# Performance work log

Hardware: AMD Instinct MI355X
Metric: run time of the kernel (lower is better)

## Reference

```python
import jax, jax.numpy as jnp
import numpy as np

B, N, D, DEG = 1, 1024, 64, 64
K = 1.0  # Lorentz curvature parameter


def _ln(x, eps=1e-6):
    mu = jnp.mean(x, -1, keepdims=True)
    var = jnp.var(x, -1, keepdims=True)
    return (x - mu) / jnp.sqrt(var + eps)


def setup_inputs() -> dict:
    key = jax.random.key(0)
    ks = jax.random.split(key, 8)
    # valid Lorentz points: time = sqrt(||space||^2 + K)
    xs = jax.random.normal(ks[0], (B, N, D - 1), dtype=jnp.float32)
    x0 = jnp.sqrt(jnp.sum(xs ** 2, -1, keepdims=True) + K)
    x = jnp.concatenate([x0, xs], -1)
    # deterministic adjacency: node i -> (i+1..i+DEG) mod N, exactly E=N*DEG edges
    rows = np.repeat(np.arange(N), DEG)
    cols = (rows + np.tile(np.arange(1, DEG + 1), N)) % N
    adj_np = np.zeros((B, N, N), dtype=bool)
    adj_np[0, rows, cols] = True
    adj = jnp.asarray(adj_np)
    e = jax.random.normal(ks[1], (B, N, N, D), dtype=jnp.float32) * 0.1
    def lin(k, fo, fi):
        return jax.random.normal(k, (fo, fi), dtype=jnp.float32) / np.sqrt(fi).astype(np.float32)
    return dict(
        x=x, adj=adj, e=e, num_edges=B * N * DEG,
        W_edge=lin(ks[2], D, 3 * D), b_edge=jnp.zeros((D,), jnp.float32),
        W_node=lin(ks[3], D, 2 * D), b_node=jnp.zeros((D,), jnp.float32),
        W_hyp=lin(ks[4], D - 1, D), b_hyp=jnp.zeros((D - 1,), jnp.float32),
        W_ada=lin(ks[5], 2 * D, 1), b_ada=jnp.zeros((2 * D,), jnp.float32),
        W_adan=lin(ks[6], 3 * D, D), b_adan=jnp.zeros((3 * D,), jnp.float32),
    )


def reference(x, adj, e, num_edges, W_edge, b_edge, W_node, b_node, W_hyp, b_hyp, W_ada, b_ada, W_adan, b_adan):
    Bx, Nx, Dx = x.shape
    # manifold.logmap0 at origin o=(sqrt(K),0,..): tangent has time component 0
    x0 = x[..., :1]
    xs = x[..., 1:]
    xn = jnp.maximum(jnp.linalg.norm(xs, axis=-1, keepdims=True), 1e-7)
    u = jnp.sqrt(K) * jnp.arccosh(jnp.maximum(x0 / jnp.sqrt(K), 1.0 + 1e-7)) * xs / xn
    xt = jnp.concatenate([jnp.zeros_like(x0), u], -1)  # [B,N,D]
    # edge list (static size)
    bi, ii, jj = jnp.nonzero(adj, size=num_edges)
    hi = xt[bi, ii]          # [E,D]
    hj = xt[bi, jj]          # [E,D]
    ef = e[bi, ii, jj]       # [E,D]
    # Lorentz distance, per-edge (same math as dense cdist + gather)
    inner = -hi[:, 0] * hj[:, 0] + jnp.sum(hi[:, 1:] * hj[:, 1:], -1)
    dist = jnp.clip(jnp.sqrt(K) * jnp.arccosh(jnp.maximum(-inner / K, 1.0 + 1e-7)), 1e-6, 100.0)
    # adaLN modulation from distance: SiLU -> Linear(1, 2D)
    ada = jax.nn.silu(dist[:, None]) @ W_ada.T + b_ada      # [E,2D]
    shift, scale = jnp.split(ada, 2, axis=1)
    ei = jnp.concatenate([hi, hj, ef], -1) @ W_edge.T + b_edge  # [E,D]
    efu = _ln(ei) * (1.0 + scale) + shift                   # [E,D]
    # node model: scatter-mean by source node index into B*N slots (faithful)
    xf = xt.reshape(Bx * Nx, Dx)
    agg = jax.ops.segment_sum(efu, ii, num_segments=Bx * Nx)
    cnt = jax.ops.segment_sum(jnp.ones_like(dist), ii, num_segments=Bx * Nx)
    agg = agg / jnp.maximum(cnt, 1.0)[:, None]
    adan = jax.nn.silu(agg) @ W_adan.T + b_adan             # [B*N,3D]
    sh, sc, gate = jnp.split(adan, 3, axis=1)
    h = xf + gate * (_ln(jnp.concatenate([xf, agg], -1) @ W_node.T + b_node) * (1.0 + sc) + sh)
    # LorentzHypLinear: project space then recompute time
    sp = h @ W_hyp.T + b_hyp                                # [B*N,D-1]
    t = jnp.sqrt(jnp.sum(sp ** 2, -1, keepdims=True) + K)
    out = jnp.concatenate([t, sp], -1) * jnp.sqrt(K / K)    # manifold_out.k == manifold.k
    return out.reshape(Bx, Nx, Dx)
```

## Files before the change

kernel.cpp:

```cpp
#include <hip/hip_runtime.h>

#define N_NODES 1024
#define D 64
#define FSTRIDE 200

typedef __bf16 bf16x8 __attribute__((ext_vector_type(8)));
typedef __bf16 bf16x4 __attribute__((ext_vector_type(4)));
typedef float f32x4 __attribute__((ext_vector_type(4)));

__device__ __forceinline__ float wave_reduce_sum(float v) {
#pragma unroll
    for (int m = 32; m >= 1; m >>= 1) v += __shfl_xor(v, m, 64);
    return v;
}

__global__ __launch_bounds__(256) void prep_kernel(const float* __restrict__ W_edge,
                                                   __bf16* __restrict__ Wb) {
    int idx = blockIdx.x * 256 + threadIdx.x;
    float4 v = ((const float4*)W_edge)[idx];
    bf16x4 o = {(__bf16)v.x, (__bf16)v.y, (__bf16)v.z, (__bf16)v.w};
    ((bf16x4*)Wb)[idx] = o;
}

__global__ __launch_bounds__(64) void xt_kernel(const float* __restrict__ x,
                                                float* __restrict__ xt) {
    const int i = blockIdx.x;
    const int l = threadIdx.x;
    float v = x[i * D + l];
    float s = (l >= 1) ? v * v : 0.f;
    s = wave_reduce_sum(s);
    float xn = fmaxf(sqrtf(s), 1e-7f);
    float x0 = __shfl(v, 0, 64);
    float z = fmaxf(x0, 1.0f + 1e-7f);
    float ach = logf(z + sqrtf((z - 1.f) * (z + 1.f)));
    float u = (l >= 1) ? ach * v / xn : 0.f;
    xt[i * D + l] = u;
}

__global__ __launch_bounds__(256) void node_kernel(
    const float* __restrict__ xt, const float* __restrict__ eg,
    const __bf16* __restrict__ Wb, const float* __restrict__ b_edge,
    const float* __restrict__ W_node, const float* __restrict__ b_node,
    const float* __restrict__ W_hyp, const float* __restrict__ b_hyp,
    const float* __restrict__ W_ada, const float* __restrict__ b_ada,
    const float* __restrict__ W_adan, const float* __restrict__ b_adan,
    float* __restrict__ out) {
    __shared__ __align__(16) char smem[27392];
    __bf16* s_F = (__bf16*)smem;
    float* s_wada = (float*)(smem + 25600);
    float* s_bada = (float*)(smem + 26112);
    float* s_sd   = (float*)(smem + 26624);
    float* s_hi   = (float*)(smem + 26880);
    float* s_be   = (float*)(smem + 27136);
    float* s_aggw = (float*)smem;
    float* s_agg  = (float*)(smem + 1024);
    float* s_sagg = (float*)(smem + 1280);
    float* s_adan = (float*)(smem + 1536);
    float* s_h    = (float*)(smem + 2304);

    const int i = blockIdx.x;
    const int t = threadIdx.x;
    const int w = t >> 6;
    const int l = t & 63;
    const int m = l & 15;
    const int q = l >> 4;

    if (t < 128) { s_wada[t] = W_ada[t]; s_bada[t] = b_ada[t]; }
    if (t < 64)  { s_hi[t] = xt[i * D + t]; s_be[t] = b_edge[t]; }

    const float hvf = xt[i * D + l];
    const __bf16 hib = (__bf16)hvf;
    float prod[16];
#pragma unroll
    for (int el = 0; el < 16; ++el) {
        int e = w * 16 + el;
        int j = (i + e + 1) & (N_NODES - 1);
        float hjv = xt[j * D + l];
        float efv = eg[((size_t)i * N_NODES + j) * D + l];
        prod[el] = hvf * hjv;
        s_F[e * FSTRIDE + l]       = hib;
        s_F[e * FSTRIDE + 64 + l]  = (__bf16)hjv;
        s_F[e * FSTRIDE + 128 + l] = (__bf16)efv;
    }
#pragma unroll
    for (int el = 0; el < 16; ++el) {
#pragma unroll
        for (int msk = 32; msk >= 1; msk >>= 1)
            prod[el] += __shfl_xor(prod[el], msk, 64);
    }
#pragma unroll
    for (int el = 0; el < 16; ++el) {
        float zz = fmaxf(-prod[el], 1.0f + 1e-7f);
        float dist = logf(zz + sqrtf((zz - 1.f) * (zz + 1.f)));
        dist = fminf(fmaxf(dist, 1e-6f), 100.f);
        float sdv = dist / (1.f + expf(-dist));
        if (l == el) s_sd[w * 16 + el] = sdv;
    }
    __syncthreads();

    f32x4 acc[4] = {};
    const bf16x8* Arow = (const bf16x8*)(s_F + (w * 16 + m) * FSTRIDE);
    const bf16x8* Wb8 = (const bf16x8*)Wb;
#pragma unroll
    for (int ks = 0; ks < 6; ++ks) {
        bf16x8 af = Arow[ks * 4 + q];
#pragma unroll
        for (int nt = 0; nt < 4; ++nt) {
            bf16x8 bfr = Wb8[(nt * 16 + m) * 24 + ks * 4 + q];
            acc[nt] = __builtin_amdgcn_mfma_f32_16x16x32_bf16(af, bfr, acc[nt], 0, 0, 0);
        }
    }
    __syncthreads();

    float vv[4][4];
    float s1[4] = {0.f, 0.f, 0.f, 0.f}, s2[4] = {0.f, 0.f, 0.f, 0.f};
#pragma unroll
    for (int nt = 0; nt < 4; ++nt) {
        float be = s_be[nt * 16 + m];
#pragma unroll
        for (int r = 0; r < 4; ++r) {
            float x = acc[nt][r] + be;
            vv[nt][r] = x;
            s1[r] += x;
            s2[r] += x * x;
        }
    }
#pragma unroll
    for (int msk = 1; msk <= 8; msk <<= 1) {
#pragma unroll
        for (int r = 0; r < 4; ++r) {
            s1[r] += __shfl_xor(s1[r], msk, 64);
            s2[r] += __shfl_xor(s2[r], msk, 64);
        }
    }
    float colp[4] = {0.f, 0.f, 0.f, 0.f};
#pragma unroll
    for (int r = 0; r < 4; ++r) {
        float mu = s1[r] * (1.f / 64.f);
        float var = s2[r] * (1.f / 64.f) - mu * mu;
        float inv = 1.f / sqrtf(var + 1e-6f);
        float sd = s_sd[w * 16 + q * 4 + r];
#pragma unroll
        for (int nt = 0; nt < 4; ++nt) {
            int n = nt * 16 + m;
            float ln = (vv[nt][r] - mu) * inv;
            float scale = sd * s_wada[64 + n] + s_bada[64 + n];
            float shift = sd * s_wada[n] + s_bada[n];
            colp[nt] += ln * (1.f + scale) + shift;
        }
    }
#pragma unroll
    for (int nt = 0; nt < 4; ++nt) {
        colp[nt] += __shfl_xor(colp[nt], 16, 64);
        colp[nt] += __shfl_xor(colp[nt], 32, 64);
    }
    if (q == 0) {
#pragma unroll
        for (int nt = 0; nt < 4; ++nt) s_aggw[w * 64 + nt * 16 + m] = colp[nt];
    }
    __syncthreads();

    if (t < 64) {
        float agg = (s_aggw[t] + s_aggw[64 + t] + s_aggw[128 + t] + s_aggw[192 + t]) * (1.f / 64.f);
        s_agg[t] = agg;
        s_sagg[t] = agg / (1.f + expf(-agg));
    }
    __syncthreads();

    if (t < 192) {
        float a = b_adan[t];
        const float4* wr = (const float4*)(W_adan + t * 64);
#pragma unroll
        for (int k = 0; k < 16; ++k) {
            float4 wv = wr[k];
            a += wv.x * s_sagg[4 * k] + wv.y * s_sagg[4 * k + 1] +
                 wv.z * s_sagg[4 * k + 2] + wv.w * s_sagg[4 * k + 3];
        }
        s_adan[t] = a;
    }
    __syncthreads();

    if (w == 0) {
        float nv = b_node[l];
        const float4* wr = (const float4*)(W_node + l * 128);
#pragma unroll
        for (int k = 0; k < 16; ++k) {
            float4 wv = wr[k];
            nv += wv.x * s_hi[4 * k] + wv.y * s_hi[4 * k + 1] +
                  wv.z * s_hi[4 * k + 2] + wv.w * s_hi[4 * k + 3];
        }
#pragma unroll
        for (int k = 16; k < 32; ++k) {
            float4 wv = wr[k];
            int b = 4 * (k - 16);
            nv += wv.x * s_agg[b] + wv.y * s_agg[b + 1] +
                  wv.z * s_agg[b + 2] + wv.w * s_agg[b + 3];
        }
        float r1 = wave_reduce_sum(nv);
        float r2 = wave_reduce_sum(nv * nv);
        float mu = r1 * (1.f / 64.f);
        float var = r2 * (1.f / 64.f) - mu * mu;
        float ln = (nv - mu) / sqrtf(var + 1e-6f);
        float sh = s_adan[l], sc = s_adan[64 + l], gate = s_adan[128 + l];
        float h = s_hi[l] + gate * (ln * (1.f + sc) + sh);
        s_h[l] = h;

        float sp = 0.f;
        if (l >= 1) {
            const float4* wr2 = (const float4*)(W_hyp + (l - 1) * 64);
            sp = b_hyp[l - 1];
#pragma unroll
            for (int k = 0; k < 16; ++k) {
                float4 wv = wr2[k];
                sp += wv.x * s_h[4 * k] + wv.y * s_h[4 * k + 1] +
                      wv.z * s_h[4 * k + 2] + wv.w * s_h[4 * k + 3];
            }
        }
        float ss = wave_reduce_sum(sp * sp);
        float tt = sqrtf(ss + 1.0f);
        out[i * D + l] = (l == 0) ? tt : sp;
    }
}

extern "C" void kernel_launch(void* const* d_in, const int* in_sizes, int n_in,
                              void* d_out, int out_size, void* d_ws, size_t ws_size,
                              hipStream_t stream) {
    const float* x      = (const float*)d_in[0];
    const float* eg     = (const float*)d_in[2];
    const float* W_edge = (const float*)d_in[4];
    const float* b_edge = (const float*)d_in[5];
    const float* W_node = (const float*)d_in[6];
    const float* b_node = (const float*)d_in[7];
    const float* W_hyp  = (const float*)d_in[8];
    const float* b_hyp  = (const float*)d_in[9];
    const float* W_ada  = (const float*)d_in[10];
    const float* b_ada  = (const float*)d_in[11];
    const float* W_adan = (const float*)d_in[12];
    const float* b_adan = (const float*)d_in[13];
    float*  xt = (float*)d_ws;
    __bf16* Wb = (__bf16*)((char*)d_ws + 262144);

    prep_kernel<<<12, 256, 0, stream>>>(W_edge, Wb);
    xt_kernel<<<N_NODES, 64, 0, stream>>>(x, xt);
    node_kernel<<<N_NODES, 256, 0, stream>>>(xt, eg, Wb, b_edge, W_node, b_node,
                                             W_hyp, b_hyp, W_ada, b_ada, W_adan, b_adan,
                                             (float*)d_out);
}
```

Baseline: 353.4 us.

## Hoist per-node hi projection out of edge GEMM and fuse weight prep into xt kernel

Because hi is identical for all 64 edges of a node, its contribution W_edge[:, :64]·hi is computed once per block as a bias vector, and the MFMA GEMM shrinks from K=192 to K=128. This reduces shared-memory staging per edge row and the LDS footprint, which may allow more resident blocks. The W_edge-to-bf16 conversion is merged into the xt kernel, removing one launch. The hi contribution is now computed in fp32 scalar code using bf16 weights and an fp32 hi, so rounding differs slightly from before.

```diff
diff --git a/kernel.cpp b/kernel.cpp
--- a/kernel.cpp
+++ b/kernel.cpp
@@ -2,7 +2,7 @@
 
 #define N_NODES 1024
 #define D 64
-#define FSTRIDE 200
+#define FSTRIDE 136
 
 typedef __bf16 bf16x8 __attribute__((ext_vector_type(8)));
 typedef __bf16 bf16x4 __attribute__((ext_vector_type(4)));
@@ -14,18 +14,21 @@
     return v;
 }
 
-__global__ __launch_bounds__(256) void prep_kernel(const float* __restrict__ W_edge,
-                                                   __bf16* __restrict__ Wb) {
-    int idx = blockIdx.x * 256 + threadIdx.x;
-    float4 v = ((const float4*)W_edge)[idx];
-    bf16x4 o = {(__bf16)v.x, (__bf16)v.y, (__bf16)v.z, (__bf16)v.w};
-    ((bf16x4*)Wb)[idx] = o;
-}
-
 __global__ __launch_bounds__(64) void xt_kernel(const float* __restrict__ x,
-                                                float* __restrict__ xt) {
+                                                float* __restrict__ xt,
+                                                const float* __restrict__ W_edge,
+                                                __bf16* __restrict__ Wb) {
     const int i = blockIdx.x;
     const int l = threadIdx.x;
+    if (i < 12) {
+#pragma unroll
+        for (int r = 0; r < 4; ++r) {
+            int idx = i * 256 + r * 64 + l;
+            float4 v = ((const float4*)W_edge)[idx];
+            bf16x4 o = {(__bf16)v.x, (__bf16)v.y, (__bf16)v.z, (__bf16)v.w};
+            ((bf16x4*)Wb)[idx] = o;
+        }
+    }
     float v = x[i * D + l];
     float s = (l >= 1) ? v * v : 0.f;
     s = wave_reduce_sum(s);
@@ -45,13 +48,13 @@
     const float* __restrict__ W_ada, const float* __restrict__ b_ada,
     const float* __restrict__ W_adan, const float* __restrict__ b_adan,
     float* __restrict__ out) {
-    __shared__ __align__(16) char smem[27392];
+    __shared__ __align__(16) char smem[19456];
     __bf16* s_F = (__bf16*)smem;
-    float* s_wada = (float*)(smem + 25600);
-    float* s_bada = (float*)(smem + 26112);
-    float* s_sd   = (float*)(smem + 26624);
-    float* s_hi   = (float*)(smem + 26880);
-    float* s_be   = (float*)(smem + 27136);
+    float* s_wada = (float*)(smem + 17408);
+    float* s_bada = (float*)(smem + 17920);
+    float* s_sd   = (float*)(smem + 18432);
+    float* s_hi   = (float*)(smem + 18688);
+    float* s_base = (float*)(smem + 18944);
     float* s_aggw = (float*)smem;
     float* s_agg  = (float*)(smem + 1024);
     float* s_sagg = (float*)(smem + 1280);
@@ -66,10 +69,9 @@
     const int q = l >> 4;
 
     if (t < 128) { s_wada[t] = W_ada[t]; s_bada[t] = b_ada[t]; }
-    if (t < 64)  { s_hi[t] = xt[i * D + t]; s_be[t] = b_edge[t]; }
+    if (t < 64)  s_hi[t] = xt[i * D + t];
 
     const float hvf = xt[i * D + l];
-    const __bf16 hib = (__bf16)hvf;
     float prod[16];
 #pragma unroll
     for (int el = 0; el < 16; ++el) {
@@ -78,9 +80,19 @@
         float hjv = xt[j * D + l];
         float efv = eg[((size_t)i * N_NODES + j) * D + l];
         prod[el] = hvf * hjv;
-        s_F[e * FSTRIDE + l]       = hib;
-        s_F[e * FSTRIDE + 64 + l]  = (__bf16)hjv;
-        s_F[e * FSTRIDE + 128 + l] = (__bf16)efv;
+        s_F[e * FSTRIDE + l]      = (__bf16)hjv;
+        s_F[e * FSTRIDE + 64 + l] = (__bf16)efv;
+    }
+    if (t < 64) {
+        float acc = b_edge[t];
+        const bf16x8* wrow = (const bf16x8*)(Wb + t * 192);
+#pragma unroll
+        for (int c = 0; c < 8; ++c) {
+            bf16x8 wv = wrow[c];
+#pragma unroll
+            for (int j8 = 0; j8 < 8; ++j8) acc += (float)wv[j8] * s_hi[c * 8 + j8];
+        }
+        s_base[t] = acc;
     }
 #pragma unroll
     for (int el = 0; el < 16; ++el) {
@@ -102,11 +114,11 @@
     const bf16x8* Arow = (const bf16x8*)(s_F + (w * 16 + m) * FSTRIDE);
     const bf16x8* Wb8 = (const bf16x8*)Wb;
 #pragma unroll
-    for (int ks = 0; ks < 6; ++ks) {
+    for (int ks = 0; ks < 4; ++ks) {
         bf16x8 af = Arow[ks * 4 + q];
 #pragma unroll
         for (int nt = 0; nt < 4; ++nt) {
-            bf16x8 bfr = Wb8[(nt * 16 + m) * 24 + ks * 4 + q];
+            bf16x8 bfr = Wb8[(nt * 16 + m) * 24 + 8 + ks * 4 + q];
             acc[nt] = __builtin_amdgcn_mfma_f32_16x16x32_bf16(af, bfr, acc[nt], 0, 0, 0);
         }
     }
@@ -116,7 +128,7 @@
     float s1[4] = {0.f, 0.f, 0.f, 0.f}, s2[4] = {0.f, 0.f, 0.f, 0.f};
 #pragma unroll
     for (int nt = 0; nt < 4; ++nt) {
-        float be = s_be[nt * 16 + m];
+        float be = s_base[nt * 16 + m];
 #pragma unroll
         for (int r = 0; r < 4; ++r) {
             float x = acc[nt][r] + be;
@@ -240,8 +252,7 @@
     float*  xt = (float*)d_ws;
     __bf16* Wb = (__bf16*)((char*)d_ws + 262144);
 
-    prep_kernel<<<12, 256, 0, stream>>>(W_edge, Wb);
-    xt_kernel<<<N_NODES, 64, 0, stream>>>(x, xt);
+    xt_kernel<<<N_NODES, 64, 0, stream>>>(x, xt, W_edge, Wb);
     node_kernel<<<N_NODES, 256, 0, stream>>>(xt, eg, Wb, b_edge, W_node, b_node,
                                              W_hyp, b_hyp, W_ada, b_ada, W_adan, b_adan,
                                              (float*)d_out);
```

After: 349.5 us. Within noise of the previous version (-1.1%).
